# Kernel optimization log

Hardware: AMD Instinct MI355X
Metric: run time of the kernel (lower is better)

Reference implementation:

```python
import jax, jax.numpy as jnp
import numpy as np

N = 100000
E = 3200000
HOP = 10

def setup_inputs() -> dict:
    key = jax.random.key(0)
    ks = jax.random.split(key, 10)
    n_in, n_hid, n_out = 512, 256, 64
    x = jax.random.normal(ks[0], (N, n_in), dtype=jnp.float32)
    edge_row = jax.random.randint(ks[1], (E,), 0, N, dtype=jnp.int32)
    edge_col = jax.random.randint(ks[2], (E,), 0, N, dtype=jnp.int32)
    # row-normalized-ish positive edge values (like a transition matrix)
    edge_vals = jax.random.uniform(ks[3], (E,), dtype=jnp.float32) / 32.0
    A2 = jax.random.uniform(ks[4], (N, 1), dtype=jnp.float32)
    # xavier-ish init scaled down for numerical sanity
    W1 = jax.random.normal(ks[5], (n_in, n_hid), dtype=jnp.float32) * (2.0 / (n_in + n_hid)) ** 0.5
    b1 = jnp.zeros((n_hid,), dtype=jnp.float32)
    W3 = jax.random.normal(ks[6], (n_hid, n_hid), dtype=jnp.float32) * (2.0 / (2 * n_hid)) ** 0.5
    b3 = jnp.zeros((n_hid,), dtype=jnp.float32)
    W2 = jax.random.normal(ks[7], (n_hid, n_out), dtype=jnp.float32) * (2.0 / (n_hid + n_out)) ** 0.5
    b2 = jnp.zeros((n_out,), dtype=jnp.float32)
    return {"x": x, "edge_row": edge_row, "edge_col": edge_col, "edge_vals": edge_vals,
            "A2": A2, "W1": W1, "b1": b1, "W3": W3, "b3": b3, "W2": W2, "b2": b2}

def _spmm(edge_row, edge_col, edge_vals, h):
    # sparse [N,N] @ dense [N,F] via gather + segment_sum
    msgs = edge_vals[:, None] * h[edge_col]          # [E, F]
    return jax.ops.segment_sum(msgs, edge_row, num_segments=N)

def reference(x, edge_row, edge_col, edge_vals, A2, W1, b1, W3, b3, W2, b2):
    # dropout layers are identity at eval time
    x0 = jax.nn.relu(x @ W1 + b1)                    # [N, n_hid]
    h = x0
    for _ in range(HOP):
        h = _spmm(edge_row, edge_col, edge_vals, h) + A2 * x0
        h = jax.nn.relu(h + h @ W3 + b3)
    return h @ W2 + b2                               # [N, n_out]
```

## Files before the change

### kernel.cpp

```cpp
#include <hip/hip_runtime.h>
#include <stdint.h>


typedef unsigned short bf16_t;
typedef __attribute__((ext_vector_type(8))) short bf16x8;
typedef __attribute__((ext_vector_type(8))) unsigned short u16x8;
typedef __attribute__((ext_vector_type(4))) float f32x4;

__device__ __forceinline__ float bf2f(bf16_t u) {
    union { unsigned int i; float f; } v; v.i = ((unsigned int)u) << 16; return v.f;
}
__device__ __forceinline__ bf16_t f2bf(float f) {
    union { float f; unsigned int i; } v; v.f = f;
    unsigned int x = v.i;
    unsigned int r = (x + 0x7fffu + ((x >> 16) & 1u)) >> 16;
    return (bf16_t)r;
}

__global__ void zero_i32(int* __restrict__ p, int n) {
    int i = blockIdx.x * blockDim.x + threadIdx.x;
    if (i < n) p[i] = 0;
}

__global__ void transpose_w(const float* __restrict__ W, bf16_t* __restrict__ Wt,
                            int K, int N) {
    int i = blockIdx.x * blockDim.x + threadIdx.x;
    if (i < K * N) {
        int k = i / N, n = i % N;
        Wt[(size_t)n * K + k] = f2bf(W[i]);
    }
}

__global__ void make_w3frag(const float* __restrict__ W3, bf16_t* __restrict__ W3f) {
    int t = blockIdx.x * blockDim.x + threadIdx.x;
    int j = t & 7;
    int f = t >> 3;
    int lane = f & 63;
    int ns = (f >> 6) & 3;
    int ks = (f >> 8) & 7;
    int g = f >> 11;
    int k = ks * 32 + ((lane >> 4) << 3) + j;
    int n = g * 64 + ns * 16 + (lane & 15);
    W3f[t] = f2bf(W3[k * 256 + n]);
}

#define BIN_CHUNK 8192
#define NBMAX 392

__global__ __launch_bounds__(256)
void bin_count(const int* __restrict__ er, int* __restrict__ bcnt, int E, int N,
               int NB) {
    __shared__ int cnt[NBMAX];
    int tid = threadIdx.x;
    for (int b = tid; b < NB; b += 256) cnt[b] = 0;
    __syncthreads();
    int e0 = blockIdx.x * BIN_CHUNK;
    int n = min(BIN_CHUNK, E - e0);
    for (int i = tid; i < n; i += 256) {
        unsigned r = (unsigned)er[e0 + i];
        if (r < (unsigned)N) atomicAdd(&cnt[r >> 8], 1);
    }
    __syncthreads();
    for (int b = tid; b < NB; b += 256) {
        int c = cnt[b];
        if (c) atomicAdd(&bcnt[b], c);
    }
}

__global__ __launch_bounds__(512)
void scan_buckets(const int* __restrict__ bcnt, int* __restrict__ bucket_base,
                  int* __restrict__ bcur, int NB) {
    __shared__ int s[512];
    int t = threadIdx.x;
    int v = (t < NB) ? bcnt[t] : 0;
    s[t] = v;
    __syncthreads();
    for (int off = 1; off < 512; off <<= 1) {
        int u = (t >= off) ? s[t - off] : 0;
        __syncthreads();
        s[t] += u;
        __syncthreads();
    }
    if (t < NB) {
        int excl = s[t] - v;
        bucket_base[t] = excl;
        bcur[t] = excl;
        if (t == NB - 1) bucket_base[NB] = s[t];
    }
}

__global__ __launch_bounds__(256)
void bin_edges(const int* __restrict__ er, const int* __restrict__ ec,
               const float* __restrict__ ev, int* __restrict__ bcur,
               int2* __restrict__ binned, int E, int N, int NB) {
    __shared__ int cnt[NBMAX];
    __shared__ int resv[NBMAX];
    int tid = threadIdx.x;
    int e0 = blockIdx.x * BIN_CHUNK;
    int n = min(BIN_CHUNK, E - e0);
    for (int b = tid; b < NB; b += 256) cnt[b] = 0;
    __syncthreads();
    for (int i = tid; i < n; i += 256) {
        unsigned r = (unsigned)er[e0 + i];
        if (r < (unsigned)N) atomicAdd(&cnt[r >> 8], 1);
    }
    __syncthreads();
    for (int b = tid; b < NB; b += 256) {
        int c = cnt[b];
        resv[b] = c ? atomicAdd(&bcur[b], c) : 0;
        cnt[b] = 0;
    }
    __syncthreads();
    for (int i = tid; i < n; i += 256) {
        unsigned r = (unsigned)er[e0 + i];
        if (r < (unsigned)N) {
            unsigned c = (unsigned)ec[e0 + i];
            float v = ev[e0 + i];
            if (c >= (unsigned)N) { c = 0; v = 0.f; }
            int b = (int)(r >> 8);
            int p = resv[b] + atomicAdd(&cnt[b], 1);
            binned[p] = make_int2((int)(((r & 255u) << 17) | c), __float_as_int(v));
        }
    }
}

#define BCAP 9216
__global__ __launch_bounds__(256)
void bucket_sort(const int* __restrict__ bucket_base, int2* __restrict__ csr,
                 int* __restrict__ row_ptr, int N, int NB) {
    __shared__ int2 ent[BCAP];
    __shared__ int cnt[256];
    __shared__ int base[256];
    __shared__ int lcur[256];
    int b = blockIdx.x;
    int tid = threadIdx.x;
    int r0 = b << 8;
    int e0 = bucket_base[b];
    int e1 = bucket_base[b + 1];
    int n = e1 - e0;
    cnt[tid] = 0;
    __syncthreads();
    for (int i = tid; i < n; i += 256) {
        int2 p = csr[e0 + i];
        if (i < BCAP) ent[i] = p;
        atomicAdd(&cnt[((unsigned)p.x >> 17) & 255u], 1);
    }
    __syncthreads();
    int v0 = cnt[tid];
    for (int off = 1; off < 256; off <<= 1) {
        int u = (tid >= off) ? cnt[tid - off] : 0;
        __syncthreads();
        cnt[tid] += u;
        __syncthreads();
    }
    base[tid] = cnt[tid] - v0;
    lcur[tid] = 0;
    if (r0 + tid < N) row_ptr[r0 + tid] = e0 + cnt[tid] - v0;
    if (b == NB - 1 && tid == 255) row_ptr[N] = e1;
    __syncthreads();
    for (int i = tid; i < n; i += 256) {
        int2 p = (i < BCAP) ? ent[i] : csr[e0 + i];
        int rl = (int)(((unsigned)p.x >> 17) & 255u);
        int d = base[rl] + atomicAdd(&lcur[rl], 1);
        csr[e0 + d] = make_int2(p.x & 0x1FFFF, p.y);
    }
}

__device__ __forceinline__ void fma8(float* acc, float v, u16x8 hv) {
    #pragma unroll
    for (int k = 0; k < 8; ++k)
        acc[k] = fmaf(v, bf2f((bf16_t)hv[k]), acc[k]);
}

__global__ __launch_bounds__(256, 8)
void fused_hop(const int* __restrict__ row_ptr, const int2* __restrict__ csr,
               const bf16_t* __restrict__ hin, const bf16_t* __restrict__ x0,
               const float* __restrict__ A2, const bf16_t* __restrict__ W3f,
               const float* __restrict__ bias, bf16_t* __restrict__ hout, int M) {
    __shared__ bf16_t s_tile[32 * 256];
    const int tid = threadIdx.x;
    const int w = tid >> 6, lane = tid & 63;
    const int bm = blockIdx.x * 32;
    const int half = lane >> 5, l32 = lane & 31, fo = l32 << 3;

    for (int rr = 0; rr < 8; ++rr) {
        int lrow = w * 8 + rr;
        int row = bm + lrow;
        float acc[8];
        #pragma unroll
        for (int k = 0; k < 8; ++k) acc[k] = 0.f;
        if (row < M) {
            if (half == 0) {
                float a2 = A2[row];
                u16x8 xv = *(const u16x8*)&x0[(row << 8) + fo];
                #pragma unroll
                for (int k = 0; k < 8; ++k) acc[k] = a2 * bf2f((bf16_t)xv[k]);
            }
            int e = row_ptr[row], e1 = row_ptr[row + 1];
            int nb = (e1 - e) >> 3;
            int2 q0, q1, q2, q3;
            if (nb > 0) {
                int eb = e + half;
                q0 = csr[eb]; q1 = csr[eb + 2]; q2 = csr[eb + 4]; q3 = csr[eb + 6];
            }
            for (int b = 0; b < nb; ++b) {
                int2 p0 = q0, p1 = q1, p2 = q2, p3 = q3;
                if (b + 1 < nb) {
                    int eb = e + 8 + half;
                    q0 = csr[eb]; q1 = csr[eb + 2]; q2 = csr[eb + 4]; q3 = csr[eb + 6];
                }
                u16x8 h0 = *(const u16x8*)&hin[(p0.x << 8) + fo];
                u16x8 h1 = *(const u16x8*)&hin[(p1.x << 8) + fo];
                u16x8 h2 = *(const u16x8*)&hin[(p2.x << 8) + fo];
                u16x8 h3 = *(const u16x8*)&hin[(p3.x << 8) + fo];
                fma8(acc, __int_as_float(p0.y), h0);
                fma8(acc, __int_as_float(p1.y), h1);
                fma8(acc, __int_as_float(p2.y), h2);
                fma8(acc, __int_as_float(p3.y), h3);
                e += 8;
            }
            for (; e + 2 <= e1; e += 2) {
                int2 p = csr[e + half];
                u16x8 hv = *(const u16x8*)&hin[(p.x << 8) + fo];
                fma8(acc, __int_as_float(p.y), hv);
            }
            if (e < e1 && half == 0) {
                int2 p = csr[e];
                u16x8 hv = *(const u16x8*)&hin[(p.x << 8) + fo];
                fma8(acc, __int_as_float(p.y), hv);
            }
            #pragma unroll
            for (int k = 0; k < 8; ++k) acc[k] += __shfl_xor(acc[k], 32, 64);
        }
        if (half == 0) {
            u16x8 o;
            #pragma unroll
            for (int k = 0; k < 8; ++k) o[k] = f2bf(acc[k]);
            *(u16x8*)((char*)s_tile + lrow * 512 + ((fo << 1) ^ ((lrow & 7) << 4))) = o;
        }
    }
    __syncthreads();

    const int q = lane >> 4, l16 = lane & 15;
    const int wn = w * 64;
    const bf16x8* bf = (const bf16x8*)W3f + ((size_t)w << 11);
    f32x4 acc2[2][4] = {};
    #pragma unroll
    for (int ks = 0; ks < 8; ++ks) {
        bf16x8 afr[2], bfr[4];
        #pragma unroll
        for (int ns = 0; ns < 4; ++ns)
            bfr[ns] = bf[(ks * 4 + ns) * 64 + lane];
        #pragma unroll
        for (int ms = 0; ms < 2; ++ms) {
            int ar = ms * 16 + l16;
            afr[ms] = *(const bf16x8*)((const char*)s_tile + ar * 512 +
                       ((((ks << 5) + q * 8) << 1) ^ ((ar & 7) << 4)));
        }
        #pragma unroll
        for (int ms = 0; ms < 2; ++ms)
            #pragma unroll
            for (int ns = 0; ns < 4; ++ns)
                acc2[ms][ns] = __builtin_amdgcn_mfma_f32_16x16x32_bf16(
                    afr[ms], bfr[ns], acc2[ms][ns], 0, 0, 0);
    }

    #pragma unroll
    for (int ms = 0; ms < 2; ++ms) {
        #pragma unroll
        for (int r = 0; r < 4; ++r) {
            int lrow = ms * 16 + q * 4 + r;
            int grow = bm + lrow;
            if (grow < M) {
                #pragma unroll
                for (int ns = 0; ns < 4; ++ns) {
                    int col = wn + ns * 16 + l16;
                    float v = acc2[ms][ns][r] + bias[col];
                    v += bf2f(*(const bf16_t*)((const char*)s_tile + lrow * 512 +
                              ((col << 1) ^ ((lrow & 7) << 4))));
                    v = fmaxf(v, 0.f);
                    hout[(size_t)grow * 256 + col] = f2bf(v);
                }
            }
        }
    }
}

template <int WM, int WN, bool AF32, bool RELU, typename CT>
__global__ __launch_bounds__(256)
void mfma_gemm(const void* __restrict__ Av, const bf16_t* __restrict__ Bt,
               const float* __restrict__ bias, CT* __restrict__ C,
               int M, int K, int Nfull) {
    constexpr int TM = WM * 64;
    constexpr int TN = WN * 64;
    __shared__ bf16_t As[TM * 32];
    __shared__ bf16_t Bs[TN * 32];
    const int tid = threadIdx.x;
    const int w = tid >> 6, lane = tid & 63;
    const int q = lane >> 4, l16 = lane & 15;
    const int bm = blockIdx.x * TM;
    const int bn = blockIdx.y * TN;
    const int wm = (w % WM) * 64;
    const int wn = (w / WM) * 64;

    f32x4 acc[4][4] = {};

    for (int k0 = 0; k0 < K; k0 += 32) {
        if constexpr (AF32) {
            constexpr int TPR = 256 / TM;
            constexpr int EPT = TM / 8;
            const float* A = (const float*)Av;
            int row = tid / TPR;
            int gr = min(bm + row, M - 1);
            int off = (tid % TPR) * EPT;
            const float* src = A + (size_t)gr * K + k0 + off;
            bf16_t* dst = As + row * 32 + off;
            #pragma unroll
            for (int g = 0; g < EPT / 4; ++g) {
                float4 v = *(const float4*)(src + 4 * g);
                ushort4 u;
                u.x = f2bf(v.x); u.y = f2bf(v.y); u.z = f2bf(v.z); u.w = f2bf(v.w);
                *(ushort4*)(dst + 4 * g) = u;
            }
        } else {
            const bf16_t* A = (const bf16_t*)Av;
            #pragma unroll
            for (int r = 0; r < TM / 64; ++r) {
                int rowbase = r * 64 + w * 16;
                int row = rowbase + (lane >> 2);
                int gr = min(bm + row, M - 1);
                const bf16_t* gp = A + (size_t)gr * K + k0 + (lane & 3) * 8;
                bf16_t* lp = As + rowbase * 32 + lane * 8;
                __builtin_amdgcn_global_load_lds(
                    (const __attribute__((address_space(1))) unsigned int*)gp,
                    (__attribute__((address_space(3))) unsigned int*)lp, 16, 0, 0);
            }
        }
        #pragma unroll
        for (int r = 0; r < TN / 64; ++r) {
            int rowbase = r * 64 + w * 16;
            int row = rowbase + (lane >> 2);
            const bf16_t* gp = Bt + (size_t)(bn + row) * K + k0 + (lane & 3) * 8;
            bf16_t* lp = Bs + rowbase * 32 + lane * 8;
            __builtin_amdgcn_global_load_lds(
                (const __attribute__((address_space(1))) unsigned int*)gp,
                (__attribute__((address_space(3))) unsigned int*)lp, 16, 0, 0);
        }
        __syncthreads();

        bf16x8 afr[4], bfr[4];
        #pragma unroll
        for (int ms = 0; ms < 4; ++ms)
            afr[ms] = *(const bf16x8*)&As[(wm + ms * 16 + l16) * 32 + q * 8];
        #pragma unroll
        for (int ns = 0; ns < 4; ++ns)
            bfr[ns] = *(const bf16x8*)&Bs[(wn + ns * 16 + l16) * 32 + q * 8];
        #pragma unroll
        for (int ms = 0; ms < 4; ++ms)
            #pragma unroll
            for (int ns = 0; ns < 4; ++ns)
                acc[ms][ns] = __builtin_amdgcn_mfma_f32_16x16x32_bf16(
                    afr[ms], bfr[ns], acc[ms][ns], 0, 0, 0);
        __syncthreads();
    }

    #pragma unroll
    for (int ms = 0; ms < 4; ++ms) {
        #pragma unroll
        for (int r = 0; r < 4; ++r) {
            int row = bm + wm + ms * 16 + q * 4 + r;
            if (row < M) {
                #pragma unroll
                for (int ns = 0; ns < 4; ++ns) {
                    int col = bn + wn + ns * 16 + l16;
                    float v = acc[ms][ns][r] + bias[col];
                    if constexpr (RELU) v = fmaxf(v, 0.f);
                    if constexpr (sizeof(CT) == 2) C[(size_t)row * Nfull + col] = (CT)f2bf(v);
                    else                           C[(size_t)row * Nfull + col] = (CT)v;
                }
            }
        }
    }
}

extern "C" void kernel_launch(void* const* d_in, const int* in_sizes, int n_in,
                              void* d_out, int out_size, void* d_ws, size_t ws_size,
                              hipStream_t stream) {
    const float* x   = (const float*)d_in[0];
    const int* erow  = (const int*)d_in[1];
    const int* ecol  = (const int*)d_in[2];
    const float* ev  = (const float*)d_in[3];
    const float* A2  = (const float*)d_in[4];
    const float* W1  = (const float*)d_in[5];
    const float* b1  = (const float*)d_in[6];
    const float* W3  = (const float*)d_in[7];
    const float* b3  = (const float*)d_in[8];
    const float* W2  = (const float*)d_in[9];
    const float* b2  = (const float*)d_in[10];
    float* out = (float*)d_out;

    const int N   = in_sizes[4];
    const int E   = in_sizes[1];
    const int NIN = in_sizes[0] / N;
    const int NH  = in_sizes[6];
    const int NO  = in_sizes[10];
    if (NH != 256 || NIN != 512 || NO != 64) return;
    const int NB = (N + 255) >> 8;
    if (NB > NBMAX) return;

    char* ws = (char*)d_ws;
    size_t off = 0;
    auto alloc = [&](size_t bytes) -> void* {
        void* p = ws + off;
        off += (bytes + 255) & ~(size_t)255;
        return p;
    };
    bf16_t* x0     = (bf16_t*)alloc((size_t)N * NH * 2);
    bf16_t* hA     = (bf16_t*)alloc((size_t)N * NH * 2);
    bf16_t* hB     = (bf16_t*)alloc((size_t)N * NH * 2);
    int*   row_ptr = (int*)alloc((size_t)(N + 1) * 4);
    int*   bcnt    = (int*)alloc((size_t)NB * 4);
    int*   bbase   = (int*)alloc((size_t)(NB + 1) * 4);
    int*   bcur    = (int*)alloc((size_t)NB * 4);
    int2*  csr     = (int2*)alloc((size_t)E * 8);
    bf16_t* W1t    = (bf16_t*)alloc((size_t)NIN * NH * 2);
    bf16_t* W3f    = (bf16_t*)alloc((size_t)NH * NH * 2);
    bf16_t* W2t    = (bf16_t*)alloc((size_t)NH * NO * 2);
    if (off > ws_size) return;

    zero_i32<<<1, 512, 0, stream>>>(bcnt, NB);
    bin_count<<<(E + BIN_CHUNK - 1) / BIN_CHUNK, 256, 0, stream>>>(
        erow, bcnt, E, N, NB);
    scan_buckets<<<1, 512, 0, stream>>>(bcnt, bbase, bcur, NB);
    bin_edges<<<(E + BIN_CHUNK - 1) / BIN_CHUNK, 256, 0, stream>>>(
        erow, ecol, ev, bcur, csr, E, N, NB);
    bucket_sort<<<NB, 256, 0, stream>>>(bbase, csr, row_ptr, N, NB);
    transpose_w<<<(NIN * NH + 255) / 256, 256, 0, stream>>>(W1, W1t, NIN, NH);
    make_w3frag<<<(NH * NH + 255) / 256, 256, 0, stream>>>(W3, W3f);
    transpose_w<<<(NH * NO + 255) / 256, 256, 0, stream>>>(W2, W2t, NH, NO);

    dim3 g1((N + 63) / 64, 1);
    mfma_gemm<1, 4, true, true, bf16_t><<<g1, 256, 0, stream>>>(
        x, W1t, b1, x0, N, NIN, NH);

    const bf16_t* hin = x0;
    bf16_t* hout = hA;
    for (int hop = 0; hop < 10; ++hop) {
        fused_hop<<<(N + 31) / 32, 256, 0, stream>>>(
            row_ptr, csr, hin, x0, A2, W3f, b3, hout, N);
        hin = hout;
        hout = (hout == hA) ? hB : hA;
    }

    dim3 g2((N + 255) / 256, 1);
    mfma_gemm<4, 1, false, false, float><<<g2, 256, 0, stream>>>(
        (const void*)hin, W2t, b2, out, N, NH, NO);
}
```

Measured before the change: 3.004 ms.

## Make fused hop a persistent per-wave work-stealing kernel over 16-row chunks

Replaces the one-block-per-32-rows grid with a persistent grid of 1280 blocks. Each wave grabs 16-row chunks through a global atomic counter, with one counter per hop zeroed at setup. Each wave does its own SpMM gather and the full 16x256 W3 MFMA on its private LDS tile, so the block-wide __syncthreads is gone and uneven row degrees are balanced dynamically. In exchange, W3 fragments are reloaded per chunk by every wave, launch bounds drop occupancy to 4 blocks, and the kernel relies on per-hop counters that must start at zero.

```diff
diff --git a/kernel.cpp b/kernel.cpp
--- a/kernel.cpp
+++ b/kernel.cpp
@@ -172,114 +172,117 @@
         acc[k] = fmaf(v, bf2f((bf16_t)hv[k]), acc[k]);
 }
 
-__global__ __launch_bounds__(256, 8)
+__global__ __launch_bounds__(256, 4)
 void fused_hop(const int* __restrict__ row_ptr, const int2* __restrict__ csr,
                const bf16_t* __restrict__ hin, const bf16_t* __restrict__ x0,
                const float* __restrict__ A2, const bf16_t* __restrict__ W3f,
-               const float* __restrict__ bias, bf16_t* __restrict__ hout, int M) {
-    __shared__ bf16_t s_tile[32 * 256];
-    const int tid = threadIdx.x;
-    const int w = tid >> 6, lane = tid & 63;
-    const int bm = blockIdx.x * 32;
+               const float* __restrict__ bias, bf16_t* __restrict__ hout,
+               int* __restrict__ ctr, int M) {
+    __shared__ bf16_t s_tile[4 * 16 * 256];
+    const int w = threadIdx.x >> 6, lane = threadIdx.x & 63;
+    char* stb = (char*)s_tile + (w << 13);
     const int half = lane >> 5, l32 = lane & 31, fo = l32 << 3;
-
-    for (int rr = 0; rr < 8; ++rr) {
-        int lrow = w * 8 + rr;
-        int row = bm + lrow;
-        float acc[8];
-        #pragma unroll
-        for (int k = 0; k < 8; ++k) acc[k] = 0.f;
-        if (row < M) {
+    const int q = lane >> 4, l16 = lane & 15;
+    const int nchunk = (M + 15) >> 4;
+
+    for (;;) {
+        int chunk;
+        if (lane == 0) chunk = atomicAdd(ctr, 1);
+        chunk = __shfl(chunk, 0, 64);
+        if (chunk >= nchunk) break;
+        const int bm = chunk << 4;
+
+        for (int rr = 0; rr < 16; ++rr) {
+            int row = bm + rr;
+            float acc[8];
+            #pragma unroll
+            for (int k = 0; k < 8; ++k) acc[k] = 0.f;
+            if (row < M) {
+                if (half == 0) {
+                    float a2 = A2[row];
+                    u16x8 xv = *(const u16x8*)&x0[(row << 8) + fo];
+                    #pragma unroll
+                    for (int k = 0; k < 8; ++k) acc[k] = a2 * bf2f((bf16_t)xv[k]);
+                }
+                int e = row_ptr[row], e1 = row_ptr[row + 1];
+                int nb = (e1 - e) >> 3;
+                int2 q0, q1, q2, q3;
+                if (nb > 0) {
+                    int eb = e + half;
+                    q0 = csr[eb]; q1 = csr[eb + 2]; q2 = csr[eb + 4]; q3 = csr[eb + 6];
+                }
+                for (int b = 0; b < nb; ++b) {
+                    int2 p0 = q0, p1 = q1, p2 = q2, p3 = q3;
+                    if (b + 1 < nb) {
+                        int eb = e + 8 + half;
+                        q0 = csr[eb]; q1 = csr[eb + 2]; q2 = csr[eb + 4]; q3 = csr[eb + 6];
+                    }
+                    u16x8 h0 = *(const u16x8*)&hin[(p0.x << 8) + fo];
+                    u16x8 h1 = *(const u16x8*)&hin[(p1.x << 8) + fo];
+                    u16x8 h2 = *(const u16x8*)&hin[(p2.x << 8) + fo];
+                    u16x8 h3 = *(const u16x8*)&hin[(p3.x << 8) + fo];
+                    fma8(acc, __int_as_float(p0.y), h0);
+                    fma8(acc, __int_as_float(p1.y), h1);
+                    fma8(acc, __int_as_float(p2.y), h2);
+                    fma8(acc, __int_as_float(p3.y), h3);
+                    e += 8;
+                }
+                for (; e + 2 <= e1; e += 2) {
+                    int2 p = csr[e + half];
+                    u16x8 hv = *(const u16x8*)&hin[(p.x << 8) + fo];
+                    fma8(acc, __int_as_float(p.y), hv);
+                }
+                if (e < e1 && half == 0) {
+                    int2 p = csr[e];
+                    u16x8 hv = *(const u16x8*)&hin[(p.x << 8) + fo];
+                    fma8(acc, __int_as_float(p.y), hv);
+                }
+                #pragma unroll
+                for (int k = 0; k < 8; ++k) acc[k] += __shfl_xor(acc[k], 32, 64);
+            }
             if (half == 0) {
-                float a2 = A2[row];
-                u16x8 xv = *(const u16x8*)&x0[(row << 8) + fo];
-                #pragma unroll
-                for (int k = 0; k < 8; ++k) acc[k] = a2 * bf2f((bf16_t)xv[k]);
-            }
-            int e = row_ptr[row], e1 = row_ptr[row + 1];
-            int nb = (e1 - e) >> 3;
-            int2 q0, q1, q2, q3;
-            if (nb > 0) {
-                int eb = e + half;
-                q0 = csr[eb]; q1 = csr[eb + 2]; q2 = csr[eb + 4]; q3 = csr[eb + 6];
-            }
-            for (int b = 0; b < nb; ++b) {
-                int2 p0 = q0, p1 = q1, p2 = q2, p3 = q3;
-                if (b + 1 < nb) {
-                    int eb = e + 8 + half;
-                    q0 = csr[eb]; q1 = csr[eb + 2]; q2 = csr[eb + 4]; q3 = csr[eb + 6];
-                }
-                u16x8 h0 = *(const u16x8*)&hin[(p0.x << 8) + fo];
-                u16x8 h1 = *(const u16x8*)&hin[(p1.x << 8) + fo];
-                u16x8 h2 = *(const u16x8*)&hin[(p2.x << 8) + fo];
-                u16x8 h3 = *(const u16x8*)&hin[(p3.x << 8) + fo];
-                fma8(acc, __int_as_float(p0.y), h0);
-                fma8(acc, __int_as_float(p1.y), h1);
-                fma8(acc, __int_as_float(p2.y), h2);
-                fma8(acc, __int_as_float(p3.y), h3);
-                e += 8;
-            }
-            for (; e + 2 <= e1; e += 2) {
-                int2 p = csr[e + half];
-                u16x8 hv = *(const u16x8*)&hin[(p.x << 8) + fo];
-                fma8(acc, __int_as_float(p.y), hv);
-            }
-            if (e < e1 && half == 0) {
-                int2 p = csr[e];
-                u16x8 hv = *(const u16x8*)&hin[(p.x << 8) + fo];
-                fma8(acc, __int_as_float(p.y), hv);
-            }
-            #pragma unroll
-            for (int k = 0; k < 8; ++k) acc[k] += __shfl_xor(acc[k], 32, 64);
-        }
-        if (half == 0) {
-            u16x8 o;
-            #pragma unroll
-            for (int k = 0; k < 8; ++k) o[k] = f2bf(acc[k]);
-            *(u16x8*)((char*)s_tile + lrow * 512 + ((fo << 1) ^ ((lrow & 7) << 4))) = o;
-        }
-    }
-    __syncthreads();
-
-    const int q = lane >> 4, l16 = lane & 15;
-    const int wn = w * 64;
-    const bf16x8* bf = (const bf16x8*)W3f + ((size_t)w << 11);
-    f32x4 acc2[2][4] = {};
-    #pragma unroll
-    for (int ks = 0; ks < 8; ++ks) {
-        bf16x8 afr[2], bfr[4];
-        #pragma unroll
-        for (int ns = 0; ns < 4; ++ns)
-            bfr[ns] = bf[(ks * 4 + ns) * 64 + lane];
-        #pragma unroll
-        for (int ms = 0; ms < 2; ++ms) {
-            int ar = ms * 16 + l16;
-            afr[ms] = *(const bf16x8*)((const char*)s_tile + ar * 512 +
-                       ((((ks << 5) + q * 8) << 1) ^ ((ar & 7) << 4)));
-        }
-        #pragma unroll
-        for (int ms = 0; ms < 2; ++ms)
-            #pragma unroll
-            for (int ns = 0; ns < 4; ++ns)
-                acc2[ms][ns] = __builtin_amdgcn_mfma_f32_16x16x32_bf16(
-                    afr[ms], bfr[ns], acc2[ms][ns], 0, 0, 0);
-    }
-
-    #pragma unroll
-    for (int ms = 0; ms < 2; ++ms) {
-        #pragma unroll
-        for (int r = 0; r < 4; ++r) {
-            int lrow = ms * 16 + q * 4 + r;
-            int grow = bm + lrow;
-            if (grow < M) {
-                #pragma unroll
-                for (int ns = 0; ns < 4; ++ns) {
-                    int col = wn + ns * 16 + l16;
-                    float v = acc2[ms][ns][r] + bias[col];
-                    v += bf2f(*(const bf16_t*)((const char*)s_tile + lrow * 512 +
-                              ((col << 1) ^ ((lrow & 7) << 4))));
-                    v = fmaxf(v, 0.f);
-                    hout[(size_t)grow * 256 + col] = f2bf(v);
+                u16x8 o;
+                #pragma unroll
+                for (int k = 0; k < 8; ++k) o[k] = f2bf(acc[k]);
+                *(u16x8*)(stb + rr * 512 + ((fo << 1) ^ ((rr & 7) << 4))) = o;
+            }
+        }
+
+        bf16x8 afr[8];
+        #pragma unroll
+        for (int ks = 0; ks < 8; ++ks)
+            afr[ks] = *(const bf16x8*)(stb + l16 * 512 +
+                       ((((ks << 5) + q * 8) << 1) ^ ((l16 & 7) << 4)));
+
+        #pragma unroll
+        for (int g = 0; g < 4; ++g) {
+            const bf16x8* bf = (const bf16x8*)W3f + ((size_t)g << 11);
+            f32x4 acc2[4] = {};
+            #pragma unroll
+            for (int ks = 0; ks < 8; ++ks) {
+                bf16x8 bfr[4];
+                #pragma unroll
+                for (int ns = 0; ns < 4; ++ns)
+                    bfr[ns] = bf[(ks * 4 + ns) * 64 + lane];
+                #pragma unroll
+                for (int ns = 0; ns < 4; ++ns)
+                    acc2[ns] = __builtin_amdgcn_mfma_f32_16x16x32_bf16(
+                        afr[ks], bfr[ns], acc2[ns], 0, 0, 0);
+            }
+            #pragma unroll
+            for (int ns = 0; ns < 4; ++ns) {
+                #pragma unroll
+                for (int r = 0; r < 4; ++r) {
+                    int lrow = q * 4 + r;
+                    int grow = bm + lrow;
+                    if (grow < M) {
+                        int col = g * 64 + ns * 16 + l16;
+                        float v = acc2[ns][r] + bias[col];
+                        v += bf2f(*(const bf16_t*)(stb + lrow * 512 +
+                                  ((col << 1) ^ ((lrow & 7) << 4))));
+                        v = fmaxf(v, 0.f);
+                        hout[(size_t)grow * 256 + col] = f2bf(v);
+                    }
                 }
             }
         }
@@ -422,6 +425,7 @@
     int*   bcnt    = (int*)alloc((size_t)NB * 4);
     int*   bbase   = (int*)alloc((size_t)(NB + 1) * 4);
     int*   bcur    = (int*)alloc((size_t)NB * 4);
+    int*   hopctr  = (int*)alloc((size_t)16 * 4);
     int2*  csr     = (int2*)alloc((size_t)E * 8);
     bf16_t* W1t    = (bf16_t*)alloc((size_t)NIN * NH * 2);
     bf16_t* W3f    = (bf16_t*)alloc((size_t)NH * NH * 2);
@@ -429,6 +433,7 @@
     if (off > ws_size) return;
 
     zero_i32<<<1, 512, 0, stream>>>(bcnt, NB);
+    zero_i32<<<1, 32, 0, stream>>>(hopctr, 16);
     bin_count<<<(E + BIN_CHUNK - 1) / BIN_CHUNK, 256, 0, stream>>>(
         erow, bcnt, E, N, NB);
     scan_buckets<<<1, 512, 0, stream>>>(bcnt, bbase, bcur, NB);
@@ -446,8 +451,8 @@
     const bf16_t* hin = x0;
     bf16_t* hout = hA;
     for (int hop = 0; hop < 10; ++hop) {
-        fused_hop<<<(N + 31) / 32, 256, 0, stream>>>(
-            row_ptr, csr, hin, x0, A2, W3f, b3, hout, N);
+        fused_hop<<<1280, 256, 0, stream>>>(
+            row_ptr, csr, hin, x0, A2, W3f, b3, hout, hopctr + hop, N);
         hin = hout;
         hout = (hout == hA) ? hB : hA;
     }
```

After: 6.240 ms. +107.7%, slower.

## Interleave four rows per wave in SpMM gather and sort columns within buckets

Applied to the files above, without the earlier changes.

The fused hop kernel now processes four rows at a time per wave, round-robining 8-edge chunks across them so more independent gathers are in flight. This replaces the single-row loop with its software-prefetched CSR loads, and occupancy is lowered to make room for the larger register state. The bucket sort adds a first pass that orders entries by column block before the stable row scatter, so each row's neighbours end up roughly column-ordered and gather locality improves. This costs an extra shared-memory pass in preprocessing and more registers per thread.

```diff
diff --git a/kernel.cpp b/kernel.cpp
--- a/kernel.cpp
+++ b/kernel.cpp
@@ -129,40 +129,57 @@
 void bucket_sort(const int* __restrict__ bucket_base, int2* __restrict__ csr,
                  int* __restrict__ row_ptr, int N, int NB) {
     __shared__ int2 ent[BCAP];
-    __shared__ int cnt[256];
-    __shared__ int base[256];
-    __shared__ int lcur[256];
+    __shared__ int h1[256], c1[256], h2[256], c2[256];
     int b = blockIdx.x;
     int tid = threadIdx.x;
     int r0 = b << 8;
     int e0 = bucket_base[b];
     int e1 = bucket_base[b + 1];
     int n = e1 - e0;
-    cnt[tid] = 0;
+    h1[tid] = 0; h2[tid] = 0;
     __syncthreads();
     for (int i = tid; i < n; i += 256) {
         int2 p = csr[e0 + i];
-        if (i < BCAP) ent[i] = p;
-        atomicAdd(&cnt[((unsigned)p.x >> 17) & 255u], 1);
-    }
-    __syncthreads();
-    int v0 = cnt[tid];
+        atomicAdd(&h1[(p.x & 0x1FFFF) >> 9], 1);
+        atomicAdd(&h2[((unsigned)p.x >> 17) & 255u], 1);
+    }
+    __syncthreads();
+    int v1 = h1[tid], v2 = h2[tid];
     for (int off = 1; off < 256; off <<= 1) {
-        int u = (tid >= off) ? cnt[tid - off] : 0;
-        __syncthreads();
-        cnt[tid] += u;
-        __syncthreads();
-    }
-    base[tid] = cnt[tid] - v0;
-    lcur[tid] = 0;
-    if (r0 + tid < N) row_ptr[r0 + tid] = e0 + cnt[tid] - v0;
+        int u1 = (tid >= off) ? h1[tid - off] : 0;
+        int u2 = (tid >= off) ? h2[tid - off] : 0;
+        __syncthreads();
+        h1[tid] += u1; h2[tid] += u2;
+        __syncthreads();
+    }
+    c1[tid] = h1[tid] - v1;
+    int base2 = h2[tid] - v2;
+    c2[tid] = base2;
+    if (r0 + tid < N) row_ptr[r0 + tid] = e0 + base2;
     if (b == NB - 1 && tid == 255) row_ptr[N] = e1;
     __syncthreads();
-    for (int i = tid; i < n; i += 256) {
-        int2 p = (i < BCAP) ? ent[i] : csr[e0 + i];
-        int rl = (int)(((unsigned)p.x >> 17) & 255u);
-        int d = base[rl] + atomicAdd(&lcur[rl], 1);
-        csr[e0 + d] = make_int2(p.x & 0x1FFFF, p.y);
+    if (n <= BCAP) {
+        for (int i = tid; i < n; i += 256) {
+            int2 p = csr[e0 + i];
+            int d = atomicAdd(&c1[(p.x & 0x1FFFF) >> 9], 1);
+            ent[d] = p;
+        }
+        __syncthreads();
+        for (int i = tid; i < n; i += 256) {
+            int2 p = ent[i];
+            int d = atomicAdd(&c2[((unsigned)p.x >> 17) & 255u], 1);
+            csr[e0 + d] = make_int2(p.x & 0x1FFFF, p.y);
+        }
+    } else {
+        for (int i = tid; i < n; i += 256) {
+            if (i < BCAP) ent[i] = csr[e0 + i];
+        }
+        __syncthreads();
+        for (int i = tid; i < n; i += 256) {
+            int2 p = (i < BCAP) ? ent[i] : csr[e0 + i];
+            int d = atomicAdd(&c2[((unsigned)p.x >> 17) & 255u], 1);
+            csr[e0 + d] = make_int2(p.x & 0x1FFFF, p.y);
+        }
     }
 }
 
@@ -172,7 +189,7 @@
         acc[k] = fmaf(v, bf2f((bf16_t)hv[k]), acc[k]);
 }
 
-__global__ __launch_bounds__(256, 8)
+__global__ __launch_bounds__(256, 5)
 void fused_hop(const int* __restrict__ row_ptr, const int2* __restrict__ csr,
                const bf16_t* __restrict__ hin, const bf16_t* __restrict__ x0,
                const float* __restrict__ A2, const bf16_t* __restrict__ W3f,
@@ -183,60 +200,71 @@
     const int bm = blockIdx.x * 32;
     const int half = lane >> 5, l32 = lane & 31, fo = l32 << 3;
 
-    for (int rr = 0; rr < 8; ++rr) {
-        int lrow = w * 8 + rr;
-        int row = bm + lrow;
-        float acc[8];
-        #pragma unroll
-        for (int k = 0; k < 8; ++k) acc[k] = 0.f;
-        if (row < M) {
+    #pragma unroll
+    for (int gq = 0; gq < 2; ++gq) {
+        const int rbase = w * 8 + gq * 4;
+        float acc[4][8];
+        int e[4], e1v[4];
+        #pragma unroll
+        for (int r = 0; r < 4; ++r) {
+            #pragma unroll
+            for (int k = 0; k < 8; ++k) acc[r][k] = 0.f;
+            int row = bm + rbase + r;
+            if (row < M) {
+                e[r] = row_ptr[row];
+                e1v[r] = row_ptr[row + 1];
+                if (half == 0) {
+                    float a2 = A2[row];
+                    u16x8 xv = *(const u16x8*)&x0[(row << 8) + fo];
+                    #pragma unroll
+                    for (int k = 0; k < 8; ++k) acc[r][k] = a2 * bf2f((bf16_t)xv[k]);
+                }
+            } else { e[r] = 0; e1v[r] = 0; }
+        }
+        bool more = true;
+        while (more) {
+            more = false;
+            #pragma unroll
+            for (int r = 0; r < 4; ++r) {
+                if (e[r] + 8 <= e1v[r]) {
+                    more = true;
+                    int eb = e[r] + half;
+                    int2 p0 = csr[eb], p1 = csr[eb + 2];
+                    int2 p2 = csr[eb + 4], p3 = csr[eb + 6];
+                    u16x8 h0 = *(const u16x8*)&hin[(p0.x << 8) + fo];
+                    u16x8 h1 = *(const u16x8*)&hin[(p1.x << 8) + fo];
+                    u16x8 h2 = *(const u16x8*)&hin[(p2.x << 8) + fo];
+                    u16x8 h3 = *(const u16x8*)&hin[(p3.x << 8) + fo];
+                    fma8(acc[r], __int_as_float(p0.y), h0);
+                    fma8(acc[r], __int_as_float(p1.y), h1);
+                    fma8(acc[r], __int_as_float(p2.y), h2);
+                    fma8(acc[r], __int_as_float(p3.y), h3);
+                    e[r] += 8;
+                }
+            }
+        }
+        #pragma unroll
+        for (int r = 0; r < 4; ++r) {
+            for (; e[r] + 2 <= e1v[r]; e[r] += 2) {
+                int2 p = csr[e[r] + half];
+                u16x8 hv = *(const u16x8*)&hin[(p.x << 8) + fo];
+                fma8(acc[r], __int_as_float(p.y), hv);
+            }
+            if (e[r] < e1v[r] && half == 0) {
+                int2 p = csr[e[r]];
+                u16x8 hv = *(const u16x8*)&hin[(p.x << 8) + fo];
+                fma8(acc[r], __int_as_float(p.y), hv);
+            }
+            #pragma unroll
+            for (int k = 0; k < 8; ++k) acc[r][k] += __shfl_xor(acc[r][k], 32, 64);
             if (half == 0) {
-                float a2 = A2[row];
-                u16x8 xv = *(const u16x8*)&x0[(row << 8) + fo];
+                u16x8 o;
                 #pragma unroll
-                for (int k = 0; k < 8; ++k) acc[k] = a2 * bf2f((bf16_t)xv[k]);
-            }
-            int e = row_ptr[row], e1 = row_ptr[row + 1];
-            int nb = (e1 - e) >> 3;
-            int2 q0, q1, q2, q3;
-            if (nb > 0) {
-                int eb = e + half;
-                q0 = csr[eb]; q1 = csr[eb + 2]; q2 = csr[eb + 4]; q3 = csr[eb + 6];
-            }
-            for (int b = 0; b < nb; ++b) {
-                int2 p0 = q0, p1 = q1, p2 = q2, p3 = q3;
-                if (b + 1 < nb) {
-                    int eb = e + 8 + half;
-                    q0 = csr[eb]; q1 = csr[eb + 2]; q2 = csr[eb + 4]; q3 = csr[eb + 6];
-                }
-                u16x8 h0 = *(const u16x8*)&hin[(p0.x << 8) + fo];
-                u16x8 h1 = *(const u16x8*)&hin[(p1.x << 8) + fo];
-                u16x8 h2 = *(const u16x8*)&hin[(p2.x << 8) + fo];
-                u16x8 h3 = *(const u16x8*)&hin[(p3.x << 8) + fo];
-                fma8(acc, __int_as_float(p0.y), h0);
-                fma8(acc, __int_as_float(p1.y), h1);
-                fma8(acc, __int_as_float(p2.y), h2);
-                fma8(acc, __int_as_float(p3.y), h3);
-                e += 8;
-            }
-            for (; e + 2 <= e1; e += 2) {
-                int2 p = csr[e + half];
-                u16x8 hv = *(const u16x8*)&hin[(p.x << 8) + fo];
-                fma8(acc, __int_as_float(p.y), hv);
-            }
-            if (e < e1 && half == 0) {
-                int2 p = csr[e];
-                u16x8 hv = *(const u16x8*)&hin[(p.x << 8) + fo];
-                fma8(acc, __int_as_float(p.y), hv);
-            }
-            #pragma unroll
-            for (int k = 0; k < 8; ++k) acc[k] += __shfl_xor(acc[k], 32, 64);
-        }
-        if (half == 0) {
-            u16x8 o;
-            #pragma unroll
-            for (int k = 0; k < 8; ++k) o[k] = f2bf(acc[k]);
-            *(u16x8*)((char*)s_tile + lrow * 512 + ((fo << 1) ^ ((lrow & 7) << 4))) = o;
+                for (int k = 0; k < 8; ++k) o[k] = f2bf(acc[r][k]);
+                int lrow = rbase + r;
+                *(u16x8*)((char*)s_tile + lrow * 512 +
+                          ((fo << 1) ^ ((lrow & 7) << 4))) = o;
+            }
         }
     }
     __syncthreads();
```

New measurement: 2.988 ms. No clear change (-0.5%).
